# Kernel tuning notes

Measured on AMD Instinct MI355X. Metric: run time of the kernel, lower is better.

Reference implementation:

```python
import math
import jax, jax.numpy as jnp
import numpy as np

B, T, D = 4, 512, 512
H = 8
Dh = D // H
LMAX = 64      # max_lag_candidates
C_TOPK = 2
EPS = 1e-8


def _lag_candidates(T, Lmax):
    # evenly sampled lags in [1, T-1], per _choose_lag_candidates
    if T <= 1:
        return []
    if Lmax is None or Lmax >= T - 1:
        return list(range(1, T))
    step = max(1, (T - 1) // Lmax)
    cand = list(range(1, T, step))[:Lmax]
    if cand and cand[-1] != T - 1:
        cand[-1] = T - 1
    return cand


def _l2_norm_over_time(x):
    # x: (B,H,T,Dh); column-wise l2 norm over time axis
    n = jnp.sqrt(jnp.maximum((x * x).sum(axis=2, keepdims=True), EPS))
    return x / n


def setup_inputs() -> dict:
    key = jax.random.key(0)
    ks = jax.random.split(key, 5)
    s = 0.02
    return {
        "x": jax.random.normal(ks[0], (B, T, D), jnp.float32),
        "Wq": jax.random.normal(ks[1], (D, D), jnp.float32) * s,
        "bq": jnp.zeros((D,), jnp.float32),
        "Wk": jax.random.normal(ks[2], (D, D), jnp.float32) * s,
        "bk": jnp.zeros((D,), jnp.float32),
        "Wv": jax.random.normal(ks[3], (D, D), jnp.float32) * s,
        "bv": jnp.zeros((D,), jnp.float32),
        "Wo": jax.random.normal(ks[4], (D, D), jnp.float32) * s,
        "bo": jnp.zeros((D,), jnp.float32),
        "log_tau": jnp.zeros((), jnp.float32),
        "lambda_auto": jnp.float32(0.5),
        "beta_lag": jnp.float32(0.5),
        "log_tau_lag": jnp.zeros((), jnp.float32),
    }


def reference(x, Wq, bq, Wk, bk, Wv, bv, Wo, bo, log_tau, lambda_auto, beta_lag, log_tau_lag):
    Bx, Tx, Dx = x.shape

    def split_heads(t):
        return t.reshape(Bx, Tx, H, Dh).transpose(0, 2, 1, 3)  # (B,H,T,Dh)

    Qh = split_heads(x @ Wq + bq)
    Kh = split_heads(x @ Wk + bk)
    Vh = split_heads(x @ Wv + bv)

    Qh_hat = _l2_norm_over_time(Qh)
    Kh_hat = _l2_norm_over_time(Kh)

    tau = jnp.maximum(jnp.exp(log_tau), 1e-4)

    # instantaneous (lag-0) channel-channel attention
    cov0 = jnp.einsum('bhtd,bhtc->bhdc', Kh_hat, Qh_hat)
    att0 = jax.nn.softmax(cov0 / tau, axis=-1)
    inst = jnp.einsum('bhtd,bhdc->bhtc', Vh, att0)

    lags = _lag_candidates(Tx, LMAX)
    L = len(lags)
    k_top = max(1, int(C_TOPK * math.ceil(math.log(max(Tx, 2), 2))))
    k_top = min(k_top, L)

    lags_arr = jnp.asarray(lags, jnp.int32)             # (L,)
    t_idx = jnp.arange(Tx, dtype=jnp.int32)

    # ---- exact score over all lag candidates ----
    idx_all = (t_idx[None, :] - lags_arr[:, None]) % Tx  # (L,T)
    Kroll = Kh_hat[:, :, idx_all, :]                     # (B,H,L,T,Dh)
    cov = jnp.einsum('bhltd,bhtc->bhldc', Kroll, Qh_hat)  # (B,H,L,Dh,Dh)
    diag_abs = jnp.abs(jnp.einsum('bhldd->bhld', cov)).sum(-1)
    total_abs = jnp.abs(cov).sum((-2, -1))
    off_abs = total_abs - diag_abs
    lam = jnp.clip(lambda_auto, 0.0, 1.0)
    score = lam * diag_abs + (1.0 - lam) * off_abs       # (B,H,L)

    top_scores, top_idx = jax.lax.top_k(score, k_top)    # (B,H,k)
    top_lags = lags_arr[top_idx]                         # (B,H,k)

    # ---- gather time-shifted K,V for selected lags ----
    idx = (t_idx[None, None, None, :] - top_lags[..., None]) % Tx  # (B,H,k,T)
    idx5 = idx[..., None]                                          # (B,H,k,T,1)
    Kb = jnp.broadcast_to(Kh_hat[:, :, None], (Bx, H, k_top, Tx, Dh))
    Vb = jnp.broadcast_to(Vh[:, :, None], (Bx, H, k_top, Tx, Dh))
    rolled_K = jnp.take_along_axis(Kb, idx5, axis=3)
    rolled_V = jnp.take_along_axis(Vb, idx5, axis=3)

    cov_l = jnp.einsum('bhktd,bhtc->bhkdc', rolled_K, Qh_hat)
    att_l = jax.nn.softmax(cov_l / tau, axis=-1)
    contrib = jnp.einsum('bhktd,bhkdc->bhktc', rolled_V, att_l)

    tau_lag = jnp.maximum(jnp.exp(log_tau_lag), 1e-4)
    w = jax.nn.softmax(top_scores / tau_lag, axis=-1)[..., None, None]  # (B,H,k,1,1)
    lag_sum = (contrib * w).sum(axis=2)                  # (B,H,T,Dh)

    beta = jnp.clip(beta_lag, 0.0, 1.0)
    out_h = (1.0 - beta) * inst + beta * lag_sum
    out = out_h.transpose(0, 2, 1, 3).reshape(Bx, Tx, Dx)
    return out @ Wo + bo
```

## Files before the change

kernel.cpp:

```cpp
#include <hip/hip_runtime.h>
#include <math.h>

namespace {

typedef unsigned short u16;
typedef unsigned int   u32;
using bf16x8 = __attribute__((ext_vector_type(8))) short;
using f32x4  = __attribute__((ext_vector_type(4))) float;

constexpr int T_   = 512;
constexpr int BH   = 32;
constexpr int NLAG = 64;
constexpr int KTOP = 18;

__device__ __forceinline__ int lag_of(int li) { return (li < 63) ? (1 + 7 * li) : 511; }

__device__ __forceinline__ u16 bf16r(float f) {
  u32 u = __builtin_bit_cast(u32, f);
  u += 0x7fffu + ((u >> 16) & 1u);
  return (u16)(u >> 16);
}
__device__ __forceinline__ float bf2f(u16 h) {
  u32 u = ((u32)h) << 16;
  return __builtin_bit_cast(float, u);
}

__device__ __forceinline__ bf16x8 load_shift8(const u16* pe, int odd) {
  uint4 a = *(const uint4*)(pe);
  union { u32 u[4]; bf16x8 v; } r;
  if (odd) {
    u32 b = *(const u32*)(pe + 8);
    r.u[0] = __builtin_amdgcn_alignbit(a.y, a.x, 16);
    r.u[1] = __builtin_amdgcn_alignbit(a.z, a.y, 16);
    r.u[2] = __builtin_amdgcn_alignbit(a.w, a.z, 16);
    r.u[3] = __builtin_amdgcn_alignbit(b,   a.w, 16);
  } else {
    r.u[0] = a.x; r.u[1] = a.y; r.u[2] = a.z; r.u[3] = a.w;
  }
  return r.v;
}

__global__ __launch_bounds__(256) void k_prep_x(const float* __restrict__ x,
                                                u16* __restrict__ xh, u16* __restrict__ xl) {
  int i0 = (blockIdx.x * 256 + threadIdx.x) * 4;
  float4 v = *(const float4*)(x + i0);
  float vv[4] = {v.x, v.y, v.z, v.w};
  u16 h[4], lo[4];
#pragma unroll
  for (int e = 0; e < 4; ++e) { h[e] = bf16r(vv[e]); lo[e] = bf16r(vv[e] - bf2f(h[e])); }
  *(ushort4*)(xh + i0) = make_ushort4(h[0], h[1], h[2], h[3]);
  *(ushort4*)(xl + i0) = make_ushort4(lo[0], lo[1], lo[2], lo[3]);
}

__global__ __launch_bounds__(256) void k_prep_w(const float* __restrict__ Wq, const float* __restrict__ Wk,
                                                const float* __restrict__ Wv, const float* __restrict__ Wo,
                                                u16* __restrict__ WTh, u16* __restrict__ WTl) {
  const int z = blockIdx.z;
  const float* W = (z == 0) ? Wq : (z == 1) ? Wk : (z == 2) ? Wv : Wo;
  u16* th = WTh + (size_t)z * 262144;
  u16* tl = WTl + (size_t)z * 262144;
  __shared__ float tile[64][65];
  const int r0 = blockIdx.y * 64, c0 = blockIdx.x * 64;
#pragma unroll
  for (int j = 0; j < 16; ++j) {
    int fid = threadIdx.x + 256 * j;
    int r = fid >> 6, c = fid & 63;
    tile[r][c] = W[(size_t)(r0 + r) * 512 + c0 + c];
  }
  __syncthreads();
#pragma unroll
  for (int j = 0; j < 16; ++j) {
    int fid = threadIdx.x + 256 * j;
    int n = fid >> 6, kk = fid & 63;
    float v = tile[kk][n];
    u16 h = bf16r(v);
    th[(size_t)(c0 + n) * 512 + r0 + kk] = h;
    tl[(size_t)(c0 + n) * 512 + r0 + kk] = bf16r(v - bf2f(h));
  }
}

__global__ __launch_bounds__(256) void k_qkv(const u16* __restrict__ xh, const u16* __restrict__ xl,
                                             const u16* __restrict__ WTh, const u16* __restrict__ WTl,
                                             const float* __restrict__ bq, const float* __restrict__ bk,
                                             const float* __restrict__ bv,
                                             float* __restrict__ qo, float* __restrict__ ko, float* __restrict__ vo) {
  const int z = blockIdx.z;
  const bool split = (z < 2);
  const u16* Bh_ = WTh + (size_t)z * 262144;
  const u16* Bl_ = WTl + (size_t)z * 262144;
  const float* bias = (z == 0) ? bq : (z == 1) ? bk : bv;
  float* out = (z == 0) ? qo : (z == 1) ? ko : vo;
  const int n0 = blockIdx.x * 64, m0 = blockIdx.y * 64;
  const int l = threadIdx.x & 63, w = threadIdx.x >> 6;
  const int lr = l & 15, lk = (l >> 4) * 8;
  const int arow = m0 + 16 * w + lr;
  f32x4 acc[4];
#pragma unroll
  for (int i = 0; i < 4; ++i) { float b = bias[n0 + 16 * i + lr]; acc[i] = (f32x4){b, b, b, b}; }
  for (int ks = 0; ks < 16; ++ks) {
    const int kb2 = ks * 32 + lk;
    bf16x8 A  = *(const bf16x8*)(xh + (size_t)arow * 512 + kb2);
    bf16x8 Al = {};
    if (split) Al = *(const bf16x8*)(xl + (size_t)arow * 512 + kb2);
#pragma unroll
    for (int i = 0; i < 4; ++i) {
      bf16x8 Bf = *(const bf16x8*)(Bh_ + (size_t)(n0 + 16 * i + lr) * 512 + kb2);
      acc[i] = __builtin_amdgcn_mfma_f32_16x16x32_bf16(A, Bf, acc[i], 0, 0, 0);
      if (split) {
        bf16x8 Bl2 = *(const bf16x8*)(Bl_ + (size_t)(n0 + 16 * i + lr) * 512 + kb2);
        acc[i] = __builtin_amdgcn_mfma_f32_16x16x32_bf16(A, Bl2, acc[i], 0, 0, 0);
        acc[i] = __builtin_amdgcn_mfma_f32_16x16x32_bf16(Al, Bf, acc[i], 0, 0, 0);
      }
    }
  }
#pragma unroll
  for (int i = 0; i < 4; ++i)
#pragma unroll
    for (int r = 0; r < 4; ++r) {
      int m = m0 + 16 * w + (l >> 4) * 4 + r;
      int n = n0 + 16 * i + lr;
      int b_ = m >> 9, t = m & 511, h_ = n >> 6, dh = n & 63;
      out[(((size_t)(b_ * 8 + h_)) * 512 + t) * 64 + dh] = acc[i][r];
    }
}

__global__ __launch_bounds__(256) void k_ssq(const float* __restrict__ qf, const float* __restrict__ kf,
                                             float* __restrict__ sinv) {
  const int bh = blockIdx.x, which = blockIdx.y;
  const float* Xb = (which ? kf : qf) + (size_t)bh * T_ * 64;
  const int tid = threadIdx.x;
  __shared__ float red[256];
  float ss = 0.f;
  for (int i = 0; i < 128; ++i) { float v = Xb[tid + 256 * i]; ss += v * v; }
  red[tid] = ss;
  __syncthreads();
  if (tid < 64) {
    float s = red[tid] + red[tid + 64] + red[tid + 128] + red[tid + 192];
    sinv[which * 2048 + bh * 64 + tid] = 1.0f / sqrtf(fmaxf(s, 1e-8f));
  }
}

__global__ __launch_bounds__(256) void k_pack(const float* __restrict__ qf, const float* __restrict__ kf,
                                              const float* __restrict__ vf, const float* __restrict__ sinv,
                                              u16* __restrict__ QPh, u16* __restrict__ QPl,
                                              u16* __restrict__ KTh, u16* __restrict__ KTl,
                                              u16* __restrict__ V2) {
  const int t0 = blockIdx.x * 64, bh = blockIdx.y;
  const int tid = threadIdx.x;
  const int tc0 = blockIdx.x * 2;
  __shared__ float tile[64][65];
#pragma unroll
  for (int j = 0; j < 16; ++j) {
    int fid = tid + 256 * j;
    int r = fid >> 6, c = fid & 63;
    tile[r][c] = qf[((size_t)bh * 512 + t0 + r) * 64 + c] * sinv[bh * 64 + c];
  }
  __syncthreads();
  {
    const int l = tid >> 2, jp = (tid & 3) * 2;
    const int g = l >> 4, lr = l & 15;
#pragma unroll
    for (int s = 0; s < 8; ++s) {
      int ni = s >> 1, tcl = s & 1;
      float v0 = tile[32 * tcl + 8 * g + jp][16 * ni + lr];
      float v1 = tile[32 * tcl + 8 * g + jp + 1][16 * ni + lr];
      u16 h0 = bf16r(v0), h1 = bf16r(v1);
      u16 l0 = bf16r(v0 - bf2f(h0)), l1 = bf16r(v1 - bf2f(h1));
      size_t off = (size_t)bh * 32768 + (size_t)(ni * 16 + tc0 + tcl) * 512 + l * 8 + jp;
      *(ushort2*)(QPh + off) = make_ushort2(h0, h1);
      *(ushort2*)(QPl + off) = make_ushort2(l0, l1);
    }
  }
  __syncthreads();
#pragma unroll
  for (int j = 0; j < 16; ++j) {
    int fid = tid + 256 * j;
    int r = fid >> 6, c = fid & 63;
    tile[r][c] = kf[((size_t)bh * 512 + t0 + r) * 64 + c] * sinv[2048 + bh * 64 + c];
  }
  __syncthreads();
#pragma unroll
  for (int j = 0; j < 16; ++j) {
    int fid = tid + 256 * j;
    int c = fid >> 6, tl2 = fid & 63;
    float v = tile[tl2][c];
    u16 hh = bf16r(v);
    u16 ll = bf16r(v - bf2f(hh));
    size_t base = ((size_t)bh * 64 + c) * 1024 + t0 + tl2;
    KTh[base] = hh;       KTl[base] = ll;
    KTh[base + 512] = hh; KTl[base + 512] = ll;
  }
#pragma unroll
  for (int j = 0; j < 4; ++j) {
    int r = (tid >> 4) + 16 * j, c4 = (tid & 15) * 4;
    float4 v4 = *(const float4*)(vf + ((size_t)bh * 512 + t0 + r) * 64 + c4);
    ushort4 o = make_ushort4(bf16r(v4.x), bf16r(v4.y), bf16r(v4.z), bf16r(v4.w));
    size_t base = ((size_t)bh * 1024 + t0 + r) * 64 + c4;
    *(ushort4*)(V2 + base) = o;
    *(ushort4*)(V2 + base + 512 * 64) = o;
  }
}

__global__ __launch_bounds__(256, 2) void k_cov(const u16* __restrict__ KTh, const u16* __restrict__ KTl,
                                                const u16* __restrict__ QPh, const u16* __restrict__ QPl,
                                                float* __restrict__ cov, float* __restrict__ score,
                                                const float* __restrict__ p_lambda) {
  const int wg = blockIdx.x;
  const int xcd = wg & 7, jj = wg >> 3;
  const int bh = xcd * 4 + jj / 65;
  const int li = jj % 65;
  const int lag = (li == 0) ? 0 : lag_of(li - 1);
  const int tid = threadIdx.x, l = tid & 63, w = tid >> 6;
  const int lr = l & 15, lk = (l >> 4) * 8;
  __shared__ f32x4 lred[2][1024];
  const int shift = 512 - lag;
  const int sbase = shift & ~1;
  const int odd = shift & 1;
  const u16* qp_h = QPh + (size_t)bh * 32768 + (size_t)l * 8;
  const u16* qp_l = QPl + (size_t)bh * 32768 + (size_t)l * 8;
  const u16* kh = KTh + (size_t)bh * 65536 + (size_t)lr * 1024 + w * 128 + lk + sbase;
  const u16* kl = KTl + (size_t)bh * 65536 + (size_t)lr * 1024 + w * 128 + lk + sbase;
  f32x4 acc[4][4] = {};
#pragma unroll
  for (int kk = 0; kk < 4; ++kk) {
    const int o = kk * 32;
    const int tc = w * 4 + kk;
    bf16x8 Bh2[4], Bl2[4];
#pragma unroll
    for (int ni = 0; ni < 4; ++ni) {
      size_t soff = (size_t)(ni * 16 + tc) * 512;
      Bh2[ni] = *(const bf16x8*)(qp_h + soff);
      Bl2[ni] = *(const bf16x8*)(qp_l + soff);
    }
#pragma unroll
    for (int mi = 0; mi < 4; ++mi) {
      bf16x8 Ah = load_shift8(kh + mi * 16384 + o, odd);
      bf16x8 Al = load_shift8(kl + mi * 16384 + o, odd);
#pragma unroll
      for (int ni = 0; ni < 4; ++ni) {
        acc[mi][ni] = __builtin_amdgcn_mfma_f32_16x16x32_bf16(Ah, Bh2[ni], acc[mi][ni], 0, 0, 0);
        acc[mi][ni] = __builtin_amdgcn_mfma_f32_16x16x32_bf16(Ah, Bl2[ni], acc[mi][ni], 0, 0, 0);
        acc[mi][ni] = __builtin_amdgcn_mfma_f32_16x16x32_bf16(Al, Bh2[ni], acc[mi][ni], 0, 0, 0);
      }
    }
  }
  if (w >= 2) {
#pragma unroll
    for (int mi = 0; mi < 4; ++mi)
#pragma unroll
      for (int ni = 0; ni < 4; ++ni) lred[w - 2][(mi * 4 + ni) * 64 + l] = acc[mi][ni];
  }
  __syncthreads();
  if (w < 2) {
#pragma unroll
    for (int mi = 0; mi < 4; ++mi)
#pragma unroll
      for (int ni = 0; ni < 4; ++ni) acc[mi][ni] += lred[w][(mi * 4 + ni) * 64 + l];
  }
  __syncthreads();
  if (w == 1) {
#pragma unroll
    for (int mi = 0; mi < 4; ++mi)
#pragma unroll
      for (int ni = 0; ni < 4; ++ni) lred[0][(mi * 4 + ni) * 64 + l] = acc[mi][ni];
  }
  __syncthreads();
  if (w == 0) {
    float* cb = cov + ((size_t)li * BH + bh) * 4096;
    float labs = 0.f, ldiag = 0.f;
#pragma unroll
    for (int mi = 0; mi < 4; ++mi)
#pragma unroll
      for (int ni = 0; ni < 4; ++ni) {
        acc[mi][ni] += lred[0][(mi * 4 + ni) * 64 + l];
#pragma unroll
        for (int r = 0; r < 4; ++r) {
          int d = 16 * mi + (l >> 4) * 4 + r;
          int c = 16 * ni + lr;
          float vv = acc[mi][ni][r];
          cb[(size_t)d * 64 + c] = vv;
          labs += fabsf(vv);
          if (d == c) ldiag += fabsf(vv);
        }
      }
#pragma unroll
    for (int off = 32; off > 0; off >>= 1) {
      labs += __shfl_xor(labs, off);
      ldiag += __shfl_xor(ldiag, off);
    }
    if (l == 0 && li > 0) {
      float lam = fminf(fmaxf(p_lambda[0], 0.f), 1.f);
      score[(size_t)bh * NLAG + (li - 1)] = lam * ldiag + (1.f - lam) * (labs - ldiag);
    }
  }
}

__global__ void k_topk(const float* __restrict__ score, int* __restrict__ sel,
                       float* __restrict__ wgt, const float* __restrict__ p_log_tau_lag) {
  const int bh = blockIdx.x;
  const int lane = threadIdx.x;
  float sc = score[(size_t)bh * NLAG + lane];
  float ts[KTOP];
  int ti[KTOP];
#pragma unroll
  for (int k = 0; k < KTOP; ++k) {
    float v = sc;
    int idx = lane;
#pragma unroll
    for (int off = 32; off > 0; off >>= 1) {
      float ov = __shfl_xor(v, off);
      int oi = __shfl_xor(idx, off);
      if (ov > v || (ov == v && oi < idx)) { v = ov; idx = oi; }
    }
    ts[k] = v;
    ti[k] = idx;
    if (lane == idx) sc = -3e38f;
  }
  const float tau_lag = fmaxf(expf(p_log_tau_lag[0]), 1e-4f);
  const float mx = ts[0];
  float e[KTOP];
  float sum = 0.f;
#pragma unroll
  for (int k = 0; k < KTOP; ++k) { e[k] = expf((ts[k] - mx) / tau_lag); sum += e[k]; }
  const float rs = 1.0f / sum;
  if (lane < KTOP) {
    sel[bh * KTOP + lane] = ti[lane];
    wgt[bh * KTOP + lane] = e[lane] * rs;
  }
}

__global__ __launch_bounds__(256) void k_attsm(const float* __restrict__ cov, const int* __restrict__ sel,
                                               const float* __restrict__ wgt,
                                               u16* __restrict__ attP,
                                               const float* __restrict__ p_log_tau,
                                               const float* __restrict__ p_beta) {
  const int bh = blockIdx.x, m = blockIdx.y;
  const int slot = (m == 0) ? 0 : (1 + (sel[bh * KTOP + m - 1] & 63));
  const float beta = fminf(fmaxf(p_beta[0], 0.f), 1.f);
  const float smv = (m == 0) ? (1.f - beta) : (beta * wgt[bh * KTOP + m - 1]);
  const float itau = 1.f / fmaxf(expf(p_log_tau[0]), 1e-4f);
  const float* cb = cov + ((size_t)slot * BH + bh) * 4096;
  __shared__ float att_s[64][66];
  const int lane = threadIdx.x & 63, wv = threadIdx.x >> 6;
  for (int d = wv; d < 64; d += 4) {
    float v = cb[(size_t)d * 64 + lane] * itau;
    float mx = v;
#pragma unroll
    for (int off = 32; off > 0; off >>= 1) mx = fmaxf(mx, __shfl_xor(mx, off));
    float e = expf(v - mx);
    float sm2 = e;
#pragma unroll
    for (int off = 32; off > 0; off >>= 1) sm2 += __shfl_xor(sm2, off);
    att_s[d][lane] = (e / sm2) * smv;
  }
  __syncthreads();
  u16* th = attP + ((size_t)m * BH + bh) * 4096;
  const int l = threadIdx.x >> 2, jp = (threadIdx.x & 3) * 2;
  const int g = l >> 4, lr = l & 15;
#pragma unroll
  for (int s = 0; s < 8; ++s) {
    int ni = s >> 1, tc = s & 1;
    float v0 = att_s[32 * tc + 8 * g + jp][16 * ni + lr];
    float v1 = att_s[32 * tc + 8 * g + jp + 1][16 * ni + lr];
    *(ushort2*)(th + (size_t)(ni * 2 + tc) * 512 + l * 8 + jp) = make_ushort2(bf16r(v0), bf16r(v1));
  }
}

__global__ __launch_bounds__(256) void k_contrib(const u16* __restrict__ V2,
                                                 const u16* __restrict__ attP,
                                                 const int* __restrict__ sel,
                                                 u16* __restrict__ oh) {
  const int tt = blockIdx.x;
  const int bh = blockIdx.y;
  const int b_ = bh >> 3, h_ = bh & 7;
  const int t0 = tt * 32;
  const int tid = threadIdx.x, l = tid & 63, w = tid >> 6;
  const int lr = l & 15, lk = (l >> 4) * 8;
  __shared__ f32x4 lred[2][512];
  f32x4 acc[2][4] = {};
  const u16* Vb = V2 + (size_t)bh * 65536;
  const int mstart[5] = {0, 5, 10, 15, 19};
  for (int m = mstart[w]; m < mstart[w + 1]; ++m) {
    const int lag = (m == 0) ? 0 : lag_of(sel[bh * KTOP + m - 1] & 63);
    const u16* ab = attP + ((size_t)m * BH + bh) * 4096;
#pragma unroll
    for (int ks = 0; ks < 2; ++ks) {
      const int kb2 = ks * 32 + lk;
      bf16x8 Bf[4];
#pragma unroll
      for (int ni = 0; ni < 4; ++ni)
        Bf[ni] = *(const bf16x8*)(ab + (size_t)(ni * 2 + ks) * 512 + l * 8);
#pragma unroll
      for (int mi = 0; mi < 2; ++mi) {
        const int ub = t0 + 16 * mi + 512 - lag + lr;
        bf16x8 A = *(const bf16x8*)(Vb + (size_t)ub * 64 + kb2);
#pragma unroll
        for (int ni = 0; ni < 4; ++ni)
          acc[mi][ni] = __builtin_amdgcn_mfma_f32_16x16x32_bf16(A, Bf[ni], acc[mi][ni], 0, 0, 0);
      }
    }
  }
  if (w >= 2) {
#pragma unroll
    for (int mi = 0; mi < 2; ++mi)
#pragma unroll
      for (int ni = 0; ni < 4; ++ni) lred[w - 2][(mi * 4 + ni) * 64 + l] = acc[mi][ni];
  }
  __syncthreads();
  if (w < 2) {
#pragma unroll
    for (int mi = 0; mi < 2; ++mi)
#pragma unroll
      for (int ni = 0; ni < 4; ++ni) acc[mi][ni] += lred[w][(mi * 4 + ni) * 64 + l];
  }
  __syncthreads();
  if (w == 1) {
#pragma unroll
    for (int mi = 0; mi < 2; ++mi)
#pragma unroll
      for (int ni = 0; ni < 4; ++ni) lred[0][(mi * 4 + ni) * 64 + l] = acc[mi][ni];
  }
  __syncthreads();
  if (w == 0) {
#pragma unroll
    for (int mi = 0; mi < 2; ++mi)
#pragma unroll
      for (int ni = 0; ni < 4; ++ni) {
        acc[mi][ni] += lred[0][(mi * 4 + ni) * 64 + l];
#pragma unroll
        for (int r = 0; r < 4; ++r) {
          int t = t0 + 16 * mi + (l >> 4) * 4 + r;
          int c = 16 * ni + lr;
          oh[((size_t)b_ * 512 + t) * 512 + h_ * 64 + c] = bf16r(acc[mi][ni][r]);
        }
      }
  }
}

__global__ __launch_bounds__(256) void k_out(const u16* __restrict__ oh,
                                             const u16* __restrict__ WTh,
                                             const float* __restrict__ bo, float* __restrict__ out) {
  const u16* Bh_ = WTh + (size_t)3 * 262144;
  const int n0 = blockIdx.x * 64, m0 = blockIdx.y * 64;
  const int l = threadIdx.x & 63, w = threadIdx.x >> 6;
  const int lr = l & 15, lk = (l >> 4) * 8;
  const int arow = m0 + 16 * w + lr;
  f32x4 acc[4];
#pragma unroll
  for (int i = 0; i < 4; ++i) { float b = bo[n0 + 16 * i + lr]; acc[i] = (f32x4){b, b, b, b}; }
  for (int ks = 0; ks < 16; ++ks) {
    int kb2 = ks * 32 + lk;
    bf16x8 A = *(const bf16x8*)(oh + (size_t)arow * 512 + kb2);
#pragma unroll
    for (int i = 0; i < 4; ++i) {
      bf16x8 Bf = *(const bf16x8*)(Bh_ + (size_t)(n0 + 16 * i + lr) * 512 + kb2);
      acc[i] = __builtin_amdgcn_mfma_f32_16x16x32_bf16(A, Bf, acc[i], 0, 0, 0);
    }
  }
#pragma unroll
  for (int i = 0; i < 4; ++i)
#pragma unroll
    for (int r = 0; r < 4; ++r) {
      int m = m0 + 16 * w + (l >> 4) * 4 + r;
      int n = n0 + 16 * i + lr;
      out[(size_t)m * 512 + n] = acc[i][r];
    }
}

}

extern "C" void kernel_launch(void* const* d_in, const int* in_sizes, int n_in,
                              void* d_out, int out_size, void* d_ws, size_t ws_size,
                              hipStream_t stream) {
  (void)in_sizes; (void)n_in; (void)out_size; (void)ws_size;
  const float* x  = (const float*)d_in[0];
  const float* Wq = (const float*)d_in[1];
  const float* bq = (const float*)d_in[2];
  const float* Wk = (const float*)d_in[3];
  const float* bk = (const float*)d_in[4];
  const float* Wv = (const float*)d_in[5];
  const float* bv = (const float*)d_in[6];
  const float* Wo = (const float*)d_in[7];
  const float* bo = (const float*)d_in[8];
  const float* p_log_tau     = (const float*)d_in[9];
  const float* p_lambda      = (const float*)d_in[10];
  const float* p_beta        = (const float*)d_in[11];
  const float* p_log_tau_lag = (const float*)d_in[12];

  char* ws = (char*)d_ws;
  const size_t MB = 1ull << 20;
  u16*   xh    = (u16*)(ws + 0 * MB);
  u16*   xl    = (u16*)(ws + 2 * MB);
  u16*   WTh   = (u16*)(ws + 4 * MB);
  u16*   WTl   = (u16*)(ws + 6 * MB);
  u16*   QPh   = (u16*)(ws + 8 * MB);
  u16*   QPl   = (u16*)(ws + 10 * MB);
  u16*   KTh   = (u16*)(ws + 12 * MB);
  u16*   KTl   = (u16*)(ws + 16 * MB);
  u16*   V2    = (u16*)(ws + 20 * MB);
  float* qf    = (float*)(ws + 24 * MB);
  float* kf    = (float*)(ws + 28 * MB);
  float* vf    = (float*)(ws + 32 * MB);
  u16*   attP  = (u16*)(ws + 24 * MB);
  u16*   oh    = (u16*)(ws + 32 * MB);
  float* cov   = (float*)(ws + 36 * MB);
  float* score = (float*)(ws + 70 * MB);
  float* wgt   = (float*)(ws + 70 * MB + 16384);
  int*   sel   = (int*)(ws + 70 * MB + 32768);
  float* sinv  = (float*)(ws + 70 * MB + 49152);

  const dim3 blk(256);

  k_prep_x<<<dim3(1024), blk, 0, stream>>>(x, xh, xl);
  k_prep_w<<<dim3(8, 8, 4), blk, 0, stream>>>(Wq, Wk, Wv, Wo, WTh, WTl);
  k_qkv<<<dim3(8, 32, 3), blk, 0, stream>>>(xh, xl, WTh, WTl, bq, bk, bv, qf, kf, vf);
  k_ssq<<<dim3(32, 2), blk, 0, stream>>>(qf, kf, sinv);
  k_pack<<<dim3(8, 32), blk, 0, stream>>>(qf, kf, vf, sinv, QPh, QPl, KTh, KTl, V2);
  k_cov<<<dim3(2080), blk, 0, stream>>>(KTh, KTl, QPh, QPl, cov, score, p_lambda);
  k_topk<<<dim3(32), dim3(64), 0, stream>>>(score, sel, wgt, p_log_tau_lag);
  k_attsm<<<dim3(32, 19), blk, 0, stream>>>(cov, sel, wgt, attP, p_log_tau, p_beta);
  k_contrib<<<dim3(16, 32), blk, 0, stream>>>(V2, attP, sel, oh);
  k_out<<<dim3(8, 32), blk, 0, stream>>>(oh, WTh, bo, (float*)d_out);
}
```

Before: 268.0 us.

## Interleave K hi/lo planes and store covariance in MFMA fragment layout

K's bf16 high and low parts are now stored interleaved in one buffer. The cov kernel reads both with two aligned 16-byte loads and splits them with byte permutes, which removes the odd-shift realignment path. Covariance tiles are written in native MFMA accumulator order as vector stores, and the softmax kernel reads that layout directly, doing row reductions with 16-lane shuffles instead of an LDS transpose. The cost is that the pair of loads may be unaligned for odd shifts, and the cov buffer layout now couples the two kernels.

```diff
diff --git a/kernel.cpp b/kernel.cpp
--- a/kernel.cpp
+++ b/kernel.cpp
@@ -23,21 +23,6 @@
 __device__ __forceinline__ float bf2f(u16 h) {
   u32 u = ((u32)h) << 16;
   return __builtin_bit_cast(float, u);
-}
-
-__device__ __forceinline__ bf16x8 load_shift8(const u16* pe, int odd) {
-  uint4 a = *(const uint4*)(pe);
-  union { u32 u[4]; bf16x8 v; } r;
-  if (odd) {
-    u32 b = *(const u32*)(pe + 8);
-    r.u[0] = __builtin_amdgcn_alignbit(a.y, a.x, 16);
-    r.u[1] = __builtin_amdgcn_alignbit(a.z, a.y, 16);
-    r.u[2] = __builtin_amdgcn_alignbit(a.w, a.z, 16);
-    r.u[3] = __builtin_amdgcn_alignbit(b,   a.w, 16);
-  } else {
-    r.u[0] = a.x; r.u[1] = a.y; r.u[2] = a.z; r.u[3] = a.w;
-  }
-  return r.v;
 }
 
 __global__ __launch_bounds__(256) void k_prep_x(const float* __restrict__ x,
@@ -143,7 +128,7 @@
 __global__ __launch_bounds__(256) void k_pack(const float* __restrict__ qf, const float* __restrict__ kf,
                                               const float* __restrict__ vf, const float* __restrict__ sinv,
                                               u16* __restrict__ QPh, u16* __restrict__ QPl,
-                                              u16* __restrict__ KTh, u16* __restrict__ KTl,
+                                              u16* __restrict__ KT2,
                                               u16* __restrict__ V2) {
   const int t0 = blockIdx.x * 64, bh = blockIdx.y;
   const int tid = threadIdx.x;
@@ -187,8 +172,8 @@
     u16 hh = bf16r(v);
     u16 ll = bf16r(v - bf2f(hh));
     size_t base = ((size_t)bh * 64 + c) * 1024 + t0 + tl2;
-    KTh[base] = hh;       KTl[base] = ll;
-    KTh[base + 512] = hh; KTl[base + 512] = ll;
+    *(ushort2*)(KT2 + 2 * base) = make_ushort2(hh, ll);
+    *(ushort2*)(KT2 + 2 * (base + 512)) = make_ushort2(hh, ll);
   }
 #pragma unroll
   for (int j = 0; j < 4; ++j) {
@@ -201,7 +186,7 @@
   }
 }
 
-__global__ __launch_bounds__(256, 2) void k_cov(const u16* __restrict__ KTh, const u16* __restrict__ KTl,
+__global__ __launch_bounds__(256, 2) void k_cov(const u16* __restrict__ KT2,
                                                 const u16* __restrict__ QPh, const u16* __restrict__ QPl,
                                                 float* __restrict__ cov, float* __restrict__ score,
                                                 const float* __restrict__ p_lambda) {
@@ -214,12 +199,9 @@
   const int lr = l & 15, lk = (l >> 4) * 8;
   __shared__ f32x4 lred[2][1024];
   const int shift = 512 - lag;
-  const int sbase = shift & ~1;
-  const int odd = shift & 1;
   const u16* qp_h = QPh + (size_t)bh * 32768 + (size_t)l * 8;
   const u16* qp_l = QPl + (size_t)bh * 32768 + (size_t)l * 8;
-  const u16* kh = KTh + (size_t)bh * 65536 + (size_t)lr * 1024 + w * 128 + lk + sbase;
-  const u16* kl = KTl + (size_t)bh * 65536 + (size_t)lr * 1024 + w * 128 + lk + sbase;
+  const u16* k2 = KT2 + 2 * (((size_t)bh * 64 + lr) * 1024 + (size_t)(shift + w * 128 + lk));
   f32x4 acc[4][4] = {};
 #pragma unroll
   for (int kk = 0; kk < 4; ++kk) {
@@ -234,13 +216,23 @@
     }
 #pragma unroll
     for (int mi = 0; mi < 4; ++mi) {
-      bf16x8 Ah = load_shift8(kh + mi * 16384 + o, odd);
-      bf16x8 Al = load_shift8(kl + mi * 16384 + o, odd);
+      const u16* pa = k2 + (size_t)mi * 32768 + 2 * o;
+      uint4 a = *(const uint4*)(pa);
+      uint4 b = *(const uint4*)(pa + 8);
+      union { u32 u[4]; bf16x8 v; } Ah, Al;
+      Ah.u[0] = __builtin_amdgcn_perm(a.y, a.x, 0x05040100u);
+      Al.u[0] = __builtin_amdgcn_perm(a.y, a.x, 0x07060302u);
+      Ah.u[1] = __builtin_amdgcn_perm(a.w, a.z, 0x05040100u);
+      Al.u[1] = __builtin_amdgcn_perm(a.w, a.z, 0x07060302u);
+      Ah.u[2] = __builtin_amdgcn_perm(b.y, b.x, 0x05040100u);
+      Al.u[2] = __builtin_amdgcn_perm(b.y, b.x, 0x07060302u);
+      Ah.u[3] = __builtin_amdgcn_perm(b.w, b.z, 0x05040100u);
+      Al.u[3] = __builtin_amdgcn_perm(b.w, b.z, 0x07060302u);
 #pragma unroll
       for (int ni = 0; ni < 4; ++ni) {
-        acc[mi][ni] = __builtin_amdgcn_mfma_f32_16x16x32_bf16(Ah, Bh2[ni], acc[mi][ni], 0, 0, 0);
-        acc[mi][ni] = __builtin_amdgcn_mfma_f32_16x16x32_bf16(Ah, Bl2[ni], acc[mi][ni], 0, 0, 0);
-        acc[mi][ni] = __builtin_amdgcn_mfma_f32_16x16x32_bf16(Al, Bh2[ni], acc[mi][ni], 0, 0, 0);
+        acc[mi][ni] = __builtin_amdgcn_mfma_f32_16x16x32_bf16(Ah.v, Bh2[ni], acc[mi][ni], 0, 0, 0);
+        acc[mi][ni] = __builtin_amdgcn_mfma_f32_16x16x32_bf16(Ah.v, Bl2[ni], acc[mi][ni], 0, 0, 0);
+        acc[mi][ni] = __builtin_amdgcn_mfma_f32_16x16x32_bf16(Al.v, Bh2[ni], acc[mi][ni], 0, 0, 0);
       }
     }
   }
@@ -273,12 +265,12 @@
 #pragma unroll
       for (int ni = 0; ni < 4; ++ni) {
         acc[mi][ni] += lred[0][(mi * 4 + ni) * 64 + l];
+        *(f32x4*)(cb + (size_t)(mi * 4 + ni) * 256 + l * 4) = acc[mi][ni];
 #pragma unroll
         for (int r = 0; r < 4; ++r) {
           int d = 16 * mi + (l >> 4) * 4 + r;
           int c = 16 * ni + lr;
           float vv = acc[mi][ni][r];
-          cb[(size_t)d * 64 + c] = vv;
           labs += fabsf(vv);
           if (d == c) ldiag += fabsf(vv);
         }
@@ -340,29 +332,37 @@
   const float smv = (m == 0) ? (1.f - beta) : (beta * wgt[bh * KTOP + m - 1]);
   const float itau = 1.f / fmaxf(expf(p_log_tau[0]), 1e-4f);
   const float* cb = cov + ((size_t)slot * BH + bh) * 4096;
-  __shared__ float att_s[64][66];
-  const int lane = threadIdx.x & 63, wv = threadIdx.x >> 6;
-  for (int d = wv; d < 64; d += 4) {
-    float v = cb[(size_t)d * 64 + lane] * itau;
-    float mx = v;
-#pragma unroll
-    for (int off = 32; off > 0; off >>= 1) mx = fmaxf(mx, __shfl_xor(mx, off));
-    float e = expf(v - mx);
-    float sm2 = e;
-#pragma unroll
-    for (int off = 32; off > 0; off >>= 1) sm2 += __shfl_xor(sm2, off);
-    att_s[d][lane] = (e / sm2) * smv;
-  }
-  __syncthreads();
+  const int l = threadIdx.x & 63, wv = threadIdx.x >> 6;
+  const int g = l >> 4, lr = l & 15;
+  f32x4 a[4];
+#pragma unroll
+  for (int ni = 0; ni < 4; ++ni)
+    a[ni] = *(const f32x4*)(cb + (size_t)(wv * 4 + ni) * 256 + l * 4);
+  float ev[4][4];
+#pragma unroll
+  for (int r = 0; r < 4; ++r) {
+    float vmax = a[0][r];
+#pragma unroll
+    for (int ni = 1; ni < 4; ++ni) vmax = fmaxf(vmax, a[ni][r]);
+#pragma unroll
+    for (int off = 8; off > 0; off >>= 1) vmax = fmaxf(vmax, __shfl_xor(vmax, off));
+    float s = 0.f;
+#pragma unroll
+    for (int ni = 0; ni < 4; ++ni) { ev[ni][r] = expf((a[ni][r] - vmax) * itau); s += ev[ni][r]; }
+#pragma unroll
+    for (int off = 8; off > 0; off >>= 1) s += __shfl_xor(s, off);
+    float inv = smv / s;
+#pragma unroll
+    for (int ni = 0; ni < 4; ++ni) ev[ni][r] *= inv;
+  }
   u16* th = attP + ((size_t)m * BH + bh) * 4096;
-  const int l = threadIdx.x >> 2, jp = (threadIdx.x & 3) * 2;
-  const int g = l >> 4, lr = l & 15;
-#pragma unroll
-  for (int s = 0; s < 8; ++s) {
-    int ni = s >> 1, tc = s & 1;
-    float v0 = att_s[32 * tc + 8 * g + jp][16 * ni + lr];
-    float v1 = att_s[32 * tc + 8 * g + jp + 1][16 * ni + lr];
-    *(ushort2*)(th + (size_t)(ni * 2 + tc) * 512 + l * 8 + jp) = make_ushort2(bf16r(v0), bf16r(v1));
+  const int tc = wv >> 1;
+  const int l2 = 16 * (2 * (wv & 1) + (g >> 1)) + lr;
+  const int jb = 4 * (g & 1);
+#pragma unroll
+  for (int ni = 0; ni < 4; ++ni) {
+    ushort4 o4 = make_ushort4(bf16r(ev[ni][0]), bf16r(ev[ni][1]), bf16r(ev[ni][2]), bf16r(ev[ni][3]));
+    *(ushort4*)(th + (size_t)(ni * 2 + tc) * 512 + l2 * 8 + jb) = o4;
   }
 }
 
@@ -495,8 +495,7 @@
   u16*   WTl   = (u16*)(ws + 6 * MB);
   u16*   QPh   = (u16*)(ws + 8 * MB);
   u16*   QPl   = (u16*)(ws + 10 * MB);
-  u16*   KTh   = (u16*)(ws + 12 * MB);
-  u16*   KTl   = (u16*)(ws + 16 * MB);
+  u16*   KT2   = (u16*)(ws + 12 * MB);
   u16*   V2    = (u16*)(ws + 20 * MB);
   float* qf    = (float*)(ws + 24 * MB);
   float* kf    = (float*)(ws + 28 * MB);
@@ -515,8 +514,8 @@
   k_prep_w<<<dim3(8, 8, 4), blk, 0, stream>>>(Wq, Wk, Wv, Wo, WTh, WTl);
   k_qkv<<<dim3(8, 32, 3), blk, 0, stream>>>(xh, xl, WTh, WTl, bq, bk, bv, qf, kf, vf);
   k_ssq<<<dim3(32, 2), blk, 0, stream>>>(qf, kf, sinv);
-  k_pack<<<dim3(8, 32), blk, 0, stream>>>(qf, kf, vf, sinv, QPh, QPl, KTh, KTl, V2);
-  k_cov<<<dim3(2080), blk, 0, stream>>>(KTh, KTl, QPh, QPl, cov, score, p_lambda);
+  k_pack<<<dim3(8, 32), blk, 0, stream>>>(qf, kf, vf, sinv, QPh, QPl, KT2, V2);
+  k_cov<<<dim3(2080), blk, 0, stream>>>(KT2, QPh, QPl, cov, score, p_lambda);
   k_topk<<<dim3(32), dim3(64), 0, stream>>>(score, sel, wgt, p_log_tau_lag);
   k_attsm<<<dim3(32, 19), blk, 0, stream>>>(cov, sel, wgt, attP, p_log_tau, p_beta);
   k_contrib<<<dim3(16, 32), blk, 0, stream>>>(V2, attP, sel, oh);
```

Measured after the change: 234.4 us. 1.14x faster.
